# Performance work log

Measured on AMD Instinct MI355X. Metric: run time of the kernel, lower is better.

Reference implementation:

```python
import jax, jax.numpy as jnp
import numpy as np

# Expectation-level (value-domain) semantics of FSUMGUCell (bipolar unary computing):
#  - FSULinear (unscaled)            -> ordinary affine transform
#  - FSUAdd scaled w/ ones bitstream -> scaled hardsigmoid: (x + 1) / 2
#  - FSUMul                          -> elementwise product of bipolar values
#  - bit inversion (1 - bitstream)   -> value negation in bipolar coding
#  - FSUAdd unscaled, entry=3        -> plain 3-way sum
# Docstring: 'scalehardsigmoid is scaled addition (x+1)/2, hardtanh is direct pass'.
# Resulting math: fg = (W_f [hx;x] + b_f + 1)/2 ; fg_hx = fg*hx ;
#                 ng = W_n [fg_hx;x] + b_n ; hy = ng - fg*ng + fg*hx.


def setup_inputs() -> dict:
    key = jax.random.key(0)
    ks = jax.random.split(key, 6)
    B, I, H = 65536, 256, 512
    x = jax.random.normal(ks[0], (B, I), dtype=jnp.float32)
    hx = jax.random.normal(ks[1], (B, H), dtype=jnp.float32)
    w_f = jax.random.normal(ks[2], (H, H + I), dtype=jnp.float32)
    b_f = jax.random.normal(ks[3], (H,), dtype=jnp.float32)
    w_n = jax.random.normal(ks[4], (H, H + I), dtype=jnp.float32)
    b_n = jax.random.normal(ks[5], (H,), dtype=jnp.float32)
    return {"x": x, "hx": hx, "w_f": w_f, "b_f": b_f, "w_n": w_n, "b_n": b_n}


def reference(x, hx, w_f, b_f, w_n, b_n):
    # fg_ug_in = cat(hx, x) : [B, H+I]
    fg_ug_in = jnp.concatenate([hx, x], axis=1)
    # FSULinear (unscaled): affine
    fg_in = jnp.einsum('bk,hk->bh', fg_ug_in, w_f) + b_f
    # scaled FSUAdd with ones bitstream == scaled hardsigmoid (x+1)/2
    fg = (fg_in + 1.0) * 0.5
    # static FSUMul with hx buffer: fg * hx
    fg_hx = fg * hx
    # new-gate linear on cat(fg_hx, x)
    ng_ug_in = jnp.concatenate([fg_hx, x], axis=1)
    ng = jnp.einsum('bk,hk->bh', ng_ug_in, w_n) + b_n
    # fg_ng = fg * ng ; bipolar bit inversion => value negation
    fg_ng = fg * ng
    # unscaled 3-entry FSUAdd: ng + (-fg_ng) + fg_hx
    hy = ng - fg_ng + fg_hx
    return hy
```

## Files before the change

### kernel.cpp

```cpp
#include <hip/hip_runtime.h>
#include <stdint.h>

typedef short bf16x8 __attribute__((ext_vector_type(8)));
typedef float f32x4  __attribute__((ext_vector_type(4)));

__device__ __forceinline__ uint16_t f2bf(float f) {
  uint32_t u = __builtin_bit_cast(uint32_t, f);
  u += 0x7fffu + ((u >> 16) & 1u);
  return (uint16_t)(u >> 16);
}
__device__ __forceinline__ float bf2f(uint16_t h) {
  uint32_t u = ((uint32_t)h) << 16;
  return __builtin_bit_cast(float, u);
}

__global__ void convw_kernel(const float* __restrict__ wf,
                             const float* __restrict__ wn,
                             uint16_t* __restrict__ o) {
  int i4 = (blockIdx.x * 256 + threadIdx.x) * 4;
  float4 v;
  if (i4 < 393216) v = *(const float4*)(wf + i4);
  else             v = *(const float4*)(wn + (i4 - 393216));
  ushort4 b;
  b.x = f2bf(v.x); b.y = f2bf(v.y); b.z = f2bf(v.z); b.w = f2bf(v.w);
  *(ushort4*)(o + i4) = b;
}

__device__ __forceinline__ void stage_a(uint16_t* sAbuf,
                                        const float* __restrict__ x,
                                        const float* __restrict__ hx,
                                        int blockRow, int k0, int tid) {
  const int r  = tid >> 3;
  const int c4 = (tid & 7) << 2;
  const float* src; int ld, col;
  if (k0 < 512) { src = hx; ld = 512; col = k0 + c4; }
  else          { src = x;  ld = 256; col = k0 - 512 + c4; }
  float4 v = *(const float4*)(src + (size_t)(blockRow + r) * ld + col);
  ushort4 b;
  b.x = f2bf(v.x); b.y = f2bf(v.y); b.z = f2bf(v.z); b.w = f2bf(v.w);
  *(ushort4*)(sAbuf + r * 32 + c4) = b;
}

__device__ __forceinline__ void stage_b(uint16_t* sBbuf, const uint16_t* __restrict__ w,
                                        int k0, int wave, int lane) {
#pragma unroll
  for (int i = 0; i < 4; ++i) {
    int grp = i * 8 + wave;
    int h   = grp * 16 + (lane >> 2);
    int ke  = (lane & 3) * 8;
    const uint16_t* g = w + (size_t)h * 768 + k0 + ke;
    uint16_t* l = sBbuf + grp * 512;
    __builtin_amdgcn_global_load_lds(
        (const __attribute__((address_space(1))) uint32_t*)g,
        (__attribute__((address_space(3))) uint32_t*)l, 16, 0, 0);
  }
}

__device__ __forceinline__ void load_a_sa(const uint16_t* sAbuf, bf16x8 a[2],
                                          int rl, int kg, int wm) {
#pragma unroll
  for (int mf = 0; mf < 2; ++mf)
    a[mf] = *(const bf16x8*)(sAbuf + (wm * 32 + mf * 16 + rl) * 32 + kg * 8);
}
__device__ __forceinline__ void load_a_fx(const uint16_t* sFX, bf16x8 a[2],
                                          int k0, int rl, int kg, int wm) {
#pragma unroll
  for (int mf = 0; mf < 2; ++mf) {
    int row = wm * 32 + mf * 16 + rl;
    int idx = (row * 512 + k0 + kg * 8) ^ ((row & 7) << 3);
    a[mf] = *(const bf16x8*)(sFX + idx);
  }
}
__device__ __forceinline__ void mfma_core(const bf16x8 a[2], const uint16_t* sBbuf,
                                          f32x4 acc[2][8], int rl, int kg, int wn4) {
  bf16x8 b[8];
#pragma unroll
  for (int nf = 0; nf < 8; ++nf)
    b[nf] = *(const bf16x8*)(sBbuf + (wn4 * 128 + nf * 16 + rl) * 32 + kg * 8);
#pragma unroll
  for (int mf = 0; mf < 2; ++mf)
#pragma unroll
    for (int nf = 0; nf < 8; ++nf)
      acc[mf][nf] = __builtin_amdgcn_mfma_f32_16x16x32_bf16(a[mf], b[nf], acc[mf][nf], 0, 0, 0);
}

__global__ __launch_bounds__(512) void fsumgu_kernel(
    const float* __restrict__ x,  const float* __restrict__ hx,
    const float* __restrict__ bf_, const float* __restrict__ bn_,
    const uint16_t* __restrict__ wf, const uint16_t* __restrict__ wn,
    float* __restrict__ out)
{
  extern __shared__ float4 smem4[];
  char* smem = (char*)smem4;
  uint16_t* sA  = (uint16_t*)smem;
  uint16_t* sB  = (uint16_t*)(smem + 8192);
  uint16_t* sFX = (uint16_t*)(smem + 8192 + 65536);

  const int tid  = threadIdx.x;
  const int lane = tid & 63;
  const int wave = tid >> 6;
  const int wm   = wave >> 2;
  const int wn4  = wave & 3;
  const int rl   = lane & 15;
  const int kg   = lane >> 4;
  const int blockRow = blockIdx.x * 64;

  f32x4 acc1[2][8], acc2[2][8];
#pragma unroll
  for (int mf = 0; mf < 2; ++mf)
#pragma unroll
    for (int nf = 0; nf < 8; ++nf)
      acc1[mf][nf] = f32x4{0.f, 0.f, 0.f, 0.f};

  stage_a(sA, x, hx, blockRow, 0, tid);
  stage_b(sB, wf, 0, wave, lane);
  __syncthreads();
#pragma unroll 1
  for (int kt = 0; kt < 24; ++kt) {
    const int cur = kt & 1;
    if (kt < 23) {
      stage_a(sA + (cur ^ 1) * 2048,  x, hx, blockRow, (kt + 1) * 32, tid);
      stage_b(sB + (cur ^ 1) * 16384, wf, (kt + 1) * 32, wave, lane);
    }
    bf16x8 a[2];
    load_a_sa(sA + cur * 2048, a, rl, kg, wm);
    mfma_core(a, sB + cur * 16384, acc1, rl, kg, wn4);
    __syncthreads();
  }

  stage_b(sB, wn, 0, wave, lane);

#pragma unroll
  for (int nf = 0; nf < 8; ++nf) {
    const int col = wn4 * 128 + nf * 16 + rl;
    const float bfv = bf_[col];
#pragma unroll
    for (int mf = 0; mf < 2; ++mf)
#pragma unroll
      for (int r = 0; r < 4; ++r) {
        const int row = wm * 32 + mf * 16 + kg * 4 + r;
        float fg = (acc1[mf][nf][r] + bfv + 1.0f) * 0.5f;
        acc1[mf][nf][r] = fg;
        float hxv = hx[(size_t)(blockRow + row) * 512 + col];
        sFX[(row * 512 + col) ^ ((row & 7) << 3)] = f2bf(fg * hxv);
      }
  }
  __syncthreads();

#pragma unroll
  for (int mf = 0; mf < 2; ++mf)
#pragma unroll
    for (int nf = 0; nf < 8; ++nf)
      acc2[mf][nf] = f32x4{0.f, 0.f, 0.f, 0.f};

#pragma unroll 1
  for (int kt = 0; kt < 24; ++kt) {
    const int cur = kt & 1;
    const int k0  = kt * 32;
    if (kt < 23) {
      const int k1 = (kt + 1) * 32;
      if (k1 >= 512) stage_a(sA + (cur ^ 1) * 2048, x, hx, blockRow, k1, tid);
      stage_b(sB + (cur ^ 1) * 16384, wn, k1, wave, lane);
    }
    bf16x8 a[2];
    if (k0 < 512) load_a_fx(sFX, a, k0, rl, kg, wm);
    else          load_a_sa(sA + cur * 2048, a, rl, kg, wm);
    mfma_core(a, sB + cur * 16384, acc2, rl, kg, wn4);
    __syncthreads();
  }

#pragma unroll
  for (int nf = 0; nf < 8; ++nf) {
    const int col = wn4 * 128 + nf * 16 + rl;
    const float bnv = bn_[col];
#pragma unroll
    for (int mf = 0; mf < 2; ++mf)
#pragma unroll
      for (int r = 0; r < 4; ++r) {
        const int row = wm * 32 + mf * 16 + kg * 4 + r;
        float ng  = acc2[mf][nf][r] + bnv;
        float fg  = acc1[mf][nf][r];
        float fgx = bf2f(sFX[(row * 512 + col) ^ ((row & 7) << 3)]);
        out[(size_t)(blockRow + row) * 512 + col] = ng - fg * ng + fgx;
      }
  }
}

extern "C" void kernel_launch(void* const* d_in, const int* in_sizes, int n_in,
                              void* d_out, int out_size, void* d_ws, size_t ws_size,
                              hipStream_t stream) {
  const float* x   = (const float*)d_in[0];
  const float* hx  = (const float*)d_in[1];
  const float* w_f = (const float*)d_in[2];
  const float* b_f = (const float*)d_in[3];
  const float* w_n = (const float*)d_in[4];
  const float* b_n = (const float*)d_in[5];
  float* out = (float*)d_out;

  uint16_t* wbf = (uint16_t*)d_ws;

  convw_kernel<<<768, 256, 0, stream>>>(w_f, w_n, wbf);

  const size_t lds = 8192 + 65536 + 65536;
  fsumgu_kernel<<<1024, 512, lds, stream>>>(x, hx, b_f, b_n,
                                            wbf, wbf + 393216, out);
}
```

Before: 485.2 us.

## Double threads per block to 16 waves and XOR-swizzle A/B LDS tiles

Raises the block from 512 to 1024 threads, so each of 16 waves computes a 32x64 output tile instead of 32x128. Per-wave accumulators and B fragments are halved, and staging work per thread shrinks to match. It also adds an XOR swizzle on the LDS layout of the A and B k-tiles to cut bank conflicts on the bf16x8 fragment reads. The trade-off is more waves per block with less work each and more barrier participants, while LDS use stays at about 139 KB per block, so occupancy is still one block per CU.

```diff
diff --git a/kernel.cpp b/kernel.cpp
--- a/kernel.cpp
+++ b/kernel.cpp
@@ -30,25 +30,26 @@
                                         const float* __restrict__ x,
                                         const float* __restrict__ hx,
                                         int blockRow, int k0, int tid) {
-  const int r  = tid >> 3;
-  const int c4 = (tid & 7) << 2;
+  const int r  = tid >> 4;
+  const int c2 = (tid & 15) << 1;
   const float* src; int ld, col;
-  if (k0 < 512) { src = hx; ld = 512; col = k0 + c4; }
-  else          { src = x;  ld = 256; col = k0 - 512 + c4; }
-  float4 v = *(const float4*)(src + (size_t)(blockRow + r) * ld + col);
-  ushort4 b;
-  b.x = f2bf(v.x); b.y = f2bf(v.y); b.z = f2bf(v.z); b.w = f2bf(v.w);
-  *(ushort4*)(sAbuf + r * 32 + c4) = b;
+  if (k0 < 512) { src = hx; ld = 512; col = k0 + c2; }
+  else          { src = x;  ld = 256; col = k0 - 512 + c2; }
+  float2 v = *(const float2*)(src + (size_t)(blockRow + r) * ld + col);
+  ushort2 b;
+  b.x = f2bf(v.x); b.y = f2bf(v.y);
+  const int idx = r * 32 + (((c2 >> 3) ^ ((r >> 1) & 3)) << 3) + (c2 & 7);
+  *(ushort2*)(sAbuf + idx) = b;
 }
 
 __device__ __forceinline__ void stage_b(uint16_t* sBbuf, const uint16_t* __restrict__ w,
                                         int k0, int wave, int lane) {
 #pragma unroll
-  for (int i = 0; i < 4; ++i) {
-    int grp = i * 8 + wave;
-    int h   = grp * 16 + (lane >> 2);
-    int ke  = (lane & 3) * 8;
-    const uint16_t* g = w + (size_t)h * 768 + k0 + ke;
+  for (int i = 0; i < 2; ++i) {
+    const int grp = i * 16 + wave;
+    const int h   = grp * 16 + (lane >> 2);
+    const int sc  = (lane & 3) ^ ((lane >> 3) & 3);
+    const uint16_t* g = w + (size_t)h * 768 + k0 + sc * 8;
     uint16_t* l = sBbuf + grp * 512;
     __builtin_amdgcn_global_load_lds(
         (const __attribute__((address_space(1))) uint32_t*)g,
@@ -59,32 +60,36 @@
 __device__ __forceinline__ void load_a_sa(const uint16_t* sAbuf, bf16x8 a[2],
                                           int rl, int kg, int wm) {
 #pragma unroll
-  for (int mf = 0; mf < 2; ++mf)
-    a[mf] = *(const bf16x8*)(sAbuf + (wm * 32 + mf * 16 + rl) * 32 + kg * 8);
+  for (int mf = 0; mf < 2; ++mf) {
+    const int row = wm * 32 + mf * 16 + rl;
+    a[mf] = *(const bf16x8*)(sAbuf + row * 32 + ((kg ^ ((row >> 1) & 3)) << 3));
+  }
 }
 __device__ __forceinline__ void load_a_fx(const uint16_t* sFX, bf16x8 a[2],
                                           int k0, int rl, int kg, int wm) {
 #pragma unroll
   for (int mf = 0; mf < 2; ++mf) {
-    int row = wm * 32 + mf * 16 + rl;
-    int idx = (row * 512 + k0 + kg * 8) ^ ((row & 7) << 3);
+    const int row = wm * 32 + mf * 16 + rl;
+    const int idx = (row * 512 + k0 + kg * 8) ^ ((row & 7) << 3);
     a[mf] = *(const bf16x8*)(sFX + idx);
   }
 }
 __device__ __forceinline__ void mfma_core(const bf16x8 a[2], const uint16_t* sBbuf,
-                                          f32x4 acc[2][8], int rl, int kg, int wn4) {
-  bf16x8 b[8];
-#pragma unroll
-  for (int nf = 0; nf < 8; ++nf)
-    b[nf] = *(const bf16x8*)(sBbuf + (wn4 * 128 + nf * 16 + rl) * 32 + kg * 8);
+                                          f32x4 acc[2][4], int rl, int kg, int wn8) {
+  bf16x8 b[4];
+#pragma unroll
+  for (int nf = 0; nf < 4; ++nf) {
+    const int row = wn8 * 64 + nf * 16 + rl;
+    b[nf] = *(const bf16x8*)(sBbuf + row * 32 + ((kg ^ ((row >> 1) & 3)) << 3));
+  }
 #pragma unroll
   for (int mf = 0; mf < 2; ++mf)
 #pragma unroll
-    for (int nf = 0; nf < 8; ++nf)
+    for (int nf = 0; nf < 4; ++nf)
       acc[mf][nf] = __builtin_amdgcn_mfma_f32_16x16x32_bf16(a[mf], b[nf], acc[mf][nf], 0, 0, 0);
 }
 
-__global__ __launch_bounds__(512) void fsumgu_kernel(
+__global__ __launch_bounds__(1024, 4) void fsumgu_kernel(
     const float* __restrict__ x,  const float* __restrict__ hx,
     const float* __restrict__ bf_, const float* __restrict__ bn_,
     const uint16_t* __restrict__ wf, const uint16_t* __restrict__ wn,
@@ -99,17 +104,17 @@
   const int tid  = threadIdx.x;
   const int lane = tid & 63;
   const int wave = tid >> 6;
-  const int wm   = wave >> 2;
-  const int wn4  = wave & 3;
+  const int wm   = wave >> 3;
+  const int wn8  = wave & 7;
   const int rl   = lane & 15;
   const int kg   = lane >> 4;
   const int blockRow = blockIdx.x * 64;
 
-  f32x4 acc1[2][8], acc2[2][8];
+  f32x4 acc1[2][4], acc2[2][4];
 #pragma unroll
   for (int mf = 0; mf < 2; ++mf)
 #pragma unroll
-    for (int nf = 0; nf < 8; ++nf)
+    for (int nf = 0; nf < 4; ++nf)
       acc1[mf][nf] = f32x4{0.f, 0.f, 0.f, 0.f};
 
   stage_a(sA, x, hx, blockRow, 0, tid);
@@ -124,15 +129,15 @@
     }
     bf16x8 a[2];
     load_a_sa(sA + cur * 2048, a, rl, kg, wm);
-    mfma_core(a, sB + cur * 16384, acc1, rl, kg, wn4);
+    mfma_core(a, sB + cur * 16384, acc1, rl, kg, wn8);
     __syncthreads();
   }
 
   stage_b(sB, wn, 0, wave, lane);
 
 #pragma unroll
-  for (int nf = 0; nf < 8; ++nf) {
-    const int col = wn4 * 128 + nf * 16 + rl;
+  for (int nf = 0; nf < 4; ++nf) {
+    const int col = wn8 * 64 + nf * 16 + rl;
     const float bfv = bf_[col];
 #pragma unroll
     for (int mf = 0; mf < 2; ++mf)
@@ -150,7 +155,7 @@
 #pragma unroll
   for (int mf = 0; mf < 2; ++mf)
 #pragma unroll
-    for (int nf = 0; nf < 8; ++nf)
+    for (int nf = 0; nf < 4; ++nf)
       acc2[mf][nf] = f32x4{0.f, 0.f, 0.f, 0.f};
 
 #pragma unroll 1
@@ -165,13 +170,13 @@
     bf16x8 a[2];
     if (k0 < 512) load_a_fx(sFX, a, k0, rl, kg, wm);
     else          load_a_sa(sA + cur * 2048, a, rl, kg, wm);
-    mfma_core(a, sB + cur * 16384, acc2, rl, kg, wn4);
+    mfma_core(a, sB + cur * 16384, acc2, rl, kg, wn8);
     __syncthreads();
   }
 
 #pragma unroll
-  for (int nf = 0; nf < 8; ++nf) {
-    const int col = wn4 * 128 + nf * 16 + rl;
+  for (int nf = 0; nf < 4; ++nf) {
+    const int col = wn8 * 64 + nf * 16 + rl;
     const float bnv = bn_[col];
 #pragma unroll
     for (int mf = 0; mf < 2; ++mf)
@@ -202,6 +207,6 @@
   convw_kernel<<<768, 256, 0, stream>>>(w_f, w_n, wbf);
 
   const size_t lds = 8192 + 65536 + 65536;
-  fsumgu_kernel<<<1024, 512, lds, stream>>>(x, hx, b_f, b_n,
-                                            wbf, wbf + 393216, out);
-}
+  fsumgu_kernel<<<1024, 1024, lds, stream>>>(x, hx, b_f, b_n,
+                                             wbf, wbf + 393216, out);
+}
```

Measured after the change: 499.8 us. 3.0% more time.
